# Kernel optimization log

Measured on AMD Instinct MI355X. Metric: run time of the kernel, lower is better.

Reference implementation:

```python
import jax, jax.numpy as jnp
import numpy as np

N, H, NH, E = 1024, 128, 8, 32768
DH = H // NH


def setup_inputs() -> dict:
    key = jax.random.key(0)
    ks = jax.random.split(key, 8)
    scale = 0.02
    return {
        "x": jax.random.normal(ks[0], (N, H), jnp.float32),
        "edge_index": jax.random.randint(ks[1], (2, E), 0, N, dtype=jnp.int32),
        "edge_attr": jax.random.normal(ks[2], (E, H), jnp.float32),
        "batch": jnp.zeros((N,), jnp.int32),
        "in_proj_w": jax.random.normal(ks[3], (3 * H, H), jnp.float32) * scale,
        "in_proj_b": jax.random.normal(ks[4], (3 * H,), jnp.float32) * scale,
        "out_w": jax.random.normal(ks[5], (H, H), jnp.float32) * scale,
        "out_b": jax.random.normal(ks[6], (H,), jnp.float32) * scale,
    }


def reference(x, edge_index, edge_attr, batch, in_proj_w, in_proj_b, out_w, out_b):
    # batch is all-zeros (single graph), matching the module's .squeeze(0) usage.
    n, h = x.shape
    src, dst = edge_index[0], edge_index[1]

    # to_dense_adj with edge_attr: dense key [S=N, B=N, H]; duplicates sum (scatter-add)
    key_dense = jnp.zeros((n, n, h), x.dtype).at[src, dst].add(edge_attr)
    # adjacency for the key_padding_mask; diagonal forced unmasked
    adjacency = jnp.zeros((n, n), x.dtype).at[src, dst].add(1.0)
    mask = (adjacency == 0) & (~jnp.eye(n, dtype=bool))  # [B=N, S=N], True = masked

    wq, wk, wv = in_proj_w[:h], in_proj_w[h:2 * h], in_proj_w[2 * h:]
    bq, bk, bv = in_proj_b[:h], in_proj_b[h:2 * h], in_proj_b[2 * h:]

    q = (x @ wq.T + bq).reshape(n, NH, DH)                 # [B, nh, dh]
    k = (key_dense @ wk.T + bk).reshape(n, n, NH, DH)      # [S, B, nh, dh]
    v = (key_dense @ wv.T + bv).reshape(n, n, NH, DH)      # [S, B, nh, dh]

    scores = jnp.einsum('bnd,sbnd->bns', q, k) * (1.0 / np.sqrt(DH))  # [B, nh, S]
    scores = jnp.where(mask[:, None, :], -jnp.inf, scores)
    attn = jax.nn.softmax(scores, axis=-1)

    out = jnp.einsum('bns,sbnd->bnd', attn, v).reshape(n, h)
    return out @ out_w.T + out_b
```

## Files before the change

### kernel.cpp

```cpp
#include <hip/hip_runtime.h>

#define NN 1024
#define HD 128
#define NHEAD 8
#define DHEAD 16
#define NE 32768
#define MAXDEG 128
#define PRE 16


__global__ __launch_bounds__(256) void bucket_kernel(
    const int* __restrict__ src, const int* __restrict__ dst,
    int* __restrict__ cntIn, unsigned int* __restrict__ adjBit,
    int* __restrict__ byDst) {
  int e = blockIdx.x * 256 + threadIdx.x;
  int s = src[e], d = dst[e];
  atomicOr(&adjBit[s * 32 + (d >> 5)], 1u << (d & 31));
  int si = atomicAdd(&cntIn[d << 4], 1);
  if (si < MAXDEG) byDst[d * MAXDEG + si] = (s << 16) | e;
}

__global__ __launch_bounds__(128) void node_kernel(
    const float* __restrict__ x, const float* __restrict__ ea,
    const float* __restrict__ W, const float* __restrict__ bias,
    const float* __restrict__ Wo, const float* __restrict__ ob,
    const int* __restrict__ cntIn, const unsigned int* __restrict__ adjBit,
    const int* __restrict__ byDst, float* __restrict__ out) {
  const int b = blockIdx.x, t = threadIdx.x;
  const int w = t >> 6, lane = t & 63;
  const int hn = lane >> 3, hc = lane & 7;

  __shared__ float xs[HD], qs[HD], aos[HD];
  __shared__ float qks[NHEAD * 136];
  __shared__ unsigned int aw[32];
  __shared__ int eList[MAXDEG];
  __shared__ unsigned short ePos[MAXDEG];
  __shared__ short fIdx[MAXDEG];
  __shared__ float eDot[MAXDEG * NHEAD];
  __shared__ float eAttn[MAXDEG * NHEAD];
  __shared__ float qbv[NHEAD];
  __shared__ int nSurv, allowedCnt, ndCnt;

  if (t < 32) aw[t] = adjBit[b * 32 + t];
  if (t == 0) { nSurv = 0; ndCnt = 0; }
  xs[t] = x[(size_t)b * HD + t];
  const int degI = min(cntIn[b << 4], MAXDEG);
  __syncthreads();
  if (t == 0) aw[b >> 5] |= 1u << (b & 31);
  __syncthreads();
  if (t < 32) {
    int pc = __popc(aw[t]);
    #pragma unroll
    for (int off = 16; off; off >>= 1) pc += __shfl_xor(pc, off, 32);
    if (t == 0) allowedCnt = pc;
  }

  if (t < degI) {
    int pk = byDst[b * MAXDEG + t];
    int e = pk & 0xFFFF, s = pk >> 16;
    if ((aw[s >> 5] >> (s & 31)) & 1) {
      int k = atomicAdd(&nSurv, 1);
      eList[k] = e; ePos[k] = (unsigned short)s;
    }
  }
  {
    const float4* wr = (const float4*)(W + (size_t)t * HD);
    const float4* xv4 = (const float4*)xs;
    float acc = bias[t];
    #pragma unroll
    for (int k = 0; k < HD / 4; k++) {
      float4 wv = wr[k]; float4 xv = xv4[k];
      acc += xv.x * wv.x + xv.y * wv.y + xv.z * wv.z + xv.w * wv.w;
    }
    qs[t] = acc;
    float p = acc * bias[HD + t];
    #pragma unroll
    for (int off = 8; off; off >>= 1) p += __shfl_xor(p, off, 16);
    if ((t & 15) == 0) qbv[t >> 4] = p;
  }
  __syncthreads();

  {
    const float4* wk4 = (const float4*)(W + HD * HD);
    const int c4 = t & 31, np = t >> 5;
    float4* qks4 = (float4*)qks;
    #pragma unroll
    for (int h = 0; h < 2; h++) {
      const int n = np + h * 4;
      float4 acc = make_float4(0.f, 0.f, 0.f, 0.f);
      #pragma unroll
      for (int d = 0; d < DHEAD; d++) {
        float qv = qs[n * DHEAD + d];
        float4 wv = wk4[(n * DHEAD + d) * 32 + c4];
        acc.x += qv * wv.x; acc.y += qv * wv.y;
        acc.z += qv * wv.z; acc.w += qv * wv.w;
      }
      qks4[n * 34 + c4] = acc;
    }
  }
  __syncthreads();
  const int ns = nSurv;

  float pre[PRE];
  #pragma unroll
  for (int k = 0; k < PRE; k++) {
    int e = (k < ns) ? eList[k] : 0;
    pre[k] = ea[(size_t)e * HD + t];
  }

  float frag[16];
  #pragma unroll
  for (int i = 0; i < 16; i++) frag[i] = qks[hn * 136 + hc * 16 + i];
  for (int k = w; k < ns; k += 2) {
    const float4* ap = (const float4*)(ea + (size_t)eList[k] * HD + hc * 16);
    float p = 0.f;
    #pragma unroll
    for (int i = 0; i < 4; i++) {
      float4 av = ap[i];
      p += av.x * frag[i * 4 + 0] + av.y * frag[i * 4 + 1] +
           av.z * frag[i * 4 + 2] + av.w * frag[i * 4 + 3];
    }
    p += __shfl_xor(p, 1);
    p += __shfl_xor(p, 2);
    p += __shfl_xor(p, 4);
    if (hc == 0) eDot[k * NHEAD + hn] = p;
  }
  __syncthreads();

  if (t < ns) {
    const int my = ePos[t];
    int f = t;
    for (int j = t - 1; j >= 0; j--)
      if (ePos[j] == my) f = j;
    fIdx[t] = (short)f;
    if (f == t) {
      atomicAdd(&ndCnt, 1);
    } else {
      #pragma unroll
      for (int n = 0; n < NHEAD; n++)
        atomicAdd(&eDot[f * NHEAD + n], eDot[t * NHEAD + n]);
    }
  }
  __syncthreads();

  {
    const int n = t >> 4, l16 = t & 15;
    const int nd = ndCnt;
    const float qb = qbv[n];
    const float sb = qb * 0.25f;
    float m = sb;
    for (int k = l16; k < ns; k += 16) {
      if (fIdx[k] == k) {
        float sc = (eDot[k * NHEAD + n] + qb) * 0.25f;
        eAttn[k * NHEAD + n] = sc;
        m = fmaxf(m, sc);
      }
    }
    #pragma unroll
    for (int off = 8; off; off >>= 1) m = fmaxf(m, __shfl_xor(m, off, 16));
    float l = 0.f;
    for (int k = l16; k < ns; k += 16)
      if (fIdx[k] == k) l += expf(eAttn[k * NHEAD + n] - m);
    #pragma unroll
    for (int off = 8; off; off >>= 1) l += __shfl_xor(l, off, 16);
    l += (float)(allowedCnt - nd) * expf(sb - m);
    const float inv = 1.0f / l;
    for (int k = l16; k < ns; k += 16)
      eDot[k * NHEAD + n] = expf(eAttn[fIdx[k] * NHEAD + n] - m) * inv;
  }
  __syncthreads();

  float aggr[NHEAD];
  #pragma unroll
  for (int n = 0; n < NHEAD; n++) aggr[n] = 0.f;
  #pragma unroll
  for (int k = 0; k < PRE; k++) {
    if (k < ns) {
      const float4* ed4 = (const float4*)&eDot[k * NHEAD];
      float4 a0 = ed4[0], a1 = ed4[1];
      float av = pre[k];
      aggr[0] += a0.x * av; aggr[1] += a0.y * av;
      aggr[2] += a0.z * av; aggr[3] += a0.w * av;
      aggr[4] += a1.x * av; aggr[5] += a1.y * av;
      aggr[6] += a1.z * av; aggr[7] += a1.w * av;
    }
  }
  for (int k = PRE; k < ns; k++) {
    float av = ea[(size_t)eList[k] * HD + t];
    #pragma unroll
    for (int n = 0; n < NHEAD; n++) aggr[n] += eDot[k * NHEAD + n] * av;
  }
  __syncthreads();
  #pragma unroll
  for (int n = 0; n < NHEAD; n++) qks[n * 136 + t] = aggr[n];
  __syncthreads();

  {
    int nj = t >> 4;
    const float4* wvr = (const float4*)(W + 2 * HD * HD + (size_t)t * HD);
    const float4* ar = (const float4*)&qks[nj * 136];
    float acc = bias[2 * HD + t];
    #pragma unroll
    for (int k = 0; k < HD / 4; k++) {
      float4 wv = wvr[k]; float4 av = ar[k];
      acc += av.x * wv.x + av.y * wv.y + av.z * wv.z + av.w * wv.w;
    }
    aos[t] = acc;
  }
  __syncthreads();
  {
    const float4* wor = (const float4*)(Wo + (size_t)t * HD);
    const float4* av4 = (const float4*)aos;
    float acc2 = ob[t];
    #pragma unroll
    for (int k = 0; k < HD / 4; k++) {
      float4 wv = wor[k]; float4 av = av4[k];
      acc2 += av.x * wv.x + av.y * wv.y + av.z * wv.z + av.w * wv.w;
    }
    out[(size_t)b * HD + t] = acc2;
  }
}

extern "C" void kernel_launch(void* const* d_in, const int* in_sizes, int n_in,
                              void* d_out, int out_size, void* d_ws, size_t ws_size,
                              hipStream_t stream) {
  const float* x     = (const float*)d_in[0];
  const int*   eidx  = (const int*)d_in[1];
  const float* eattr = (const float*)d_in[2];
  const float* in_w  = (const float*)d_in[4];
  const float* in_b  = (const float*)d_in[5];
  const float* out_w = (const float*)d_in[6];
  const float* out_b = (const float*)d_in[7];
  float* out = (float*)d_out;

  const int* src = eidx;
  const int* dst = eidx + NE;

  char* ws = (char*)d_ws;
  int* cntIn            = (int*)(ws + 0);
  unsigned int* adjBit  = (unsigned int*)(ws + 65536);
  int* byDst            = (int*)(ws + 196608);

  hipMemsetAsync(ws, 0, 196608, stream);
  bucket_kernel<<<NE / 256, 256, 0, stream>>>(src, dst, cntIn, adjBit, byDst);
  node_kernel<<<NN, 128, 0, stream>>>(x, eattr, in_w, in_b, out_w, out_b,
                                      cntIn, adjBit, byDst, out);
}
```

Before: 107.2 us.

## Precompute Q and Q·Wk per node tile in prep kernel alongside edge bucketing

The per-node Q projection, the q·bk bias term and the Q·Wk folded key vectors move out of node_kernel. They are now computed by extra blocks of the bucketing kernel, 16 nodes per block, so each weight row loaded is reused across the tile. node_kernel reads the precomputed qk fragments and qbv values from workspace, which removes two matvecs and two barriers from its critical path. The cost is extra global writes and reads of a 4 MB qk buffer and more register use in the prep blocks.

```diff
diff --git a/kernel.cpp b/kernel.cpp
--- a/kernel.cpp
+++ b/kernel.cpp
@@ -7,43 +7,122 @@
 #define NE 32768
 #define MAXDEG 128
 #define PRE 16
-
-
-__global__ __launch_bounds__(256) void bucket_kernel(
+#define PTILE 16
+
+
+__global__ __launch_bounds__(256) void prep_kernel(
     const int* __restrict__ src, const int* __restrict__ dst,
     int* __restrict__ cntIn, unsigned int* __restrict__ adjBit,
-    int* __restrict__ byDst) {
-  int e = blockIdx.x * 256 + threadIdx.x;
-  int s = src[e], d = dst[e];
-  atomicOr(&adjBit[s * 32 + (d >> 5)], 1u << (d & 31));
-  int si = atomicAdd(&cntIn[d << 4], 1);
-  if (si < MAXDEG) byDst[d * MAXDEG + si] = (s << 16) | e;
+    int* __restrict__ byDst, const float* __restrict__ x,
+    const float* __restrict__ W, const float* __restrict__ bias,
+    float* __restrict__ qkAll, float* __restrict__ qbvAll) {
+  const int t = threadIdx.x;
+  if (blockIdx.x < NE / 256) {
+    int e = blockIdx.x * 256 + t;
+    int s = src[e], d = dst[e];
+    atomicOr(&adjBit[s * 32 + (d >> 5)], 1u << (d & 31));
+    int si = atomicAdd(&cntIn[d << 4], 1);
+    if (si < MAXDEG) byDst[d * MAXDEG + si] = (s << 16) | e;
+    return;
+  }
+  const int node0 = (blockIdx.x - NE / 256) * PTILE;
+  __shared__ float xT[PTILE][HD];
+  __shared__ float qT[PTILE][HD + 1];
+
+  #pragma unroll
+  for (int i = 0; i < 8; i++) {
+    int idx = i * 256 + t;
+    xT[idx >> 7][idx & 127] = x[(size_t)(node0 + (idx >> 7)) * HD + (idx & 127)];
+  }
+  __syncthreads();
+
+  {
+    const int r = t & 127, jh = t >> 7;
+    const float4* wr = (const float4*)(W + (size_t)r * HD);
+    const float bq = bias[r];
+    float acc[8];
+    #pragma unroll
+    for (int j = 0; j < 8; j++) acc[j] = bq;
+    for (int k = 0; k < HD / 4; k++) {
+      float4 wv = wr[k];
+      #pragma unroll
+      for (int j = 0; j < 8; j++) {
+        const float4 xv = *(const float4*)&xT[jh * 8 + j][k * 4];
+        acc[j] += xv.x * wv.x + xv.y * wv.y + xv.z * wv.z + xv.w * wv.w;
+      }
+    }
+    #pragma unroll
+    for (int j = 0; j < 8; j++) qT[jh * 8 + j][r] = acc[j];
+  }
+  __syncthreads();
+
+  if (t < 128) {
+    const int j = t >> 3, n = t & 7;
+    float s = 0.f;
+    #pragma unroll
+    for (int d = 0; d < DHEAD; d++) s += qT[j][n * 16 + d] * bias[HD + n * 16 + d];
+    qbvAll[(node0 + j) * NHEAD + n] = s;
+  }
+
+  {
+    const int c4 = t & 31, n = t >> 5;
+    const float4* wk4 = (const float4*)(W + HD * HD);
+    float4 acc[PTILE];
+    #pragma unroll
+    for (int j = 0; j < PTILE; j++) acc[j] = make_float4(0.f, 0.f, 0.f, 0.f);
+    #pragma unroll
+    for (int d = 0; d < DHEAD; d++) {
+      float4 wv = wk4[(n * 16 + d) * 32 + c4];
+      #pragma unroll
+      for (int j = 0; j < PTILE; j++) {
+        float qv = qT[j][n * 16 + d];
+        acc[j].x += qv * wv.x; acc[j].y += qv * wv.y;
+        acc[j].z += qv * wv.z; acc[j].w += qv * wv.w;
+      }
+    }
+    #pragma unroll
+    for (int j = 0; j < PTILE; j++) {
+      float4* out4 = (float4*)(qkAll + (size_t)(node0 + j) * 1024 + n * 128);
+      out4[c4] = acc[j];
+    }
+  }
 }
 
 __global__ __launch_bounds__(128) void node_kernel(
-    const float* __restrict__ x, const float* __restrict__ ea,
+    const float* __restrict__ ea,
     const float* __restrict__ W, const float* __restrict__ bias,
     const float* __restrict__ Wo, const float* __restrict__ ob,
     const int* __restrict__ cntIn, const unsigned int* __restrict__ adjBit,
-    const int* __restrict__ byDst, float* __restrict__ out) {
+    const int* __restrict__ byDst, const float* __restrict__ qkAll,
+    const float* __restrict__ qbvAll, float* __restrict__ out) {
   const int b = blockIdx.x, t = threadIdx.x;
   const int w = t >> 6, lane = t & 63;
   const int hn = lane >> 3, hc = lane & 7;
 
-  __shared__ float xs[HD], qs[HD], aos[HD];
-  __shared__ float qks[NHEAD * 136];
+  __shared__ float aos[HD];
+  __shared__ float aggS[NHEAD][136];
   __shared__ unsigned int aw[32];
   __shared__ int eList[MAXDEG];
   __shared__ unsigned short ePos[MAXDEG];
   __shared__ short fIdx[MAXDEG];
   __shared__ float eDot[MAXDEG * NHEAD];
   __shared__ float eAttn[MAXDEG * NHEAD];
-  __shared__ float qbv[NHEAD];
+  __shared__ float qbvS[NHEAD];
   __shared__ int nSurv, allowedCnt, ndCnt;
 
+  float frag[16];
+  {
+    const float4* qp = (const float4*)(qkAll + (size_t)b * 1024 + hn * 128 + hc * 16);
+    #pragma unroll
+    for (int i = 0; i < 4; i++) {
+      float4 v = qp[i];
+      frag[i * 4 + 0] = v.x; frag[i * 4 + 1] = v.y;
+      frag[i * 4 + 2] = v.z; frag[i * 4 + 3] = v.w;
+    }
+  }
+  if (t < NHEAD) qbvS[t] = qbvAll[b * NHEAD + t];
   if (t < 32) aw[t] = adjBit[b * 32 + t];
   if (t == 0) { nSurv = 0; ndCnt = 0; }
-  xs[t] = x[(size_t)b * HD + t];
   const int degI = min(cntIn[b << 4], MAXDEG);
   __syncthreads();
   if (t == 0) aw[b >> 5] |= 1u << (b & 31);
@@ -54,7 +133,6 @@
     for (int off = 16; off; off >>= 1) pc += __shfl_xor(pc, off, 32);
     if (t == 0) allowedCnt = pc;
   }
-
   if (t < degI) {
     int pk = byDst[b * MAXDEG + t];
     int e = pk & 0xFFFF, s = pk >> 16;
@@ -63,41 +141,6 @@
       eList[k] = e; ePos[k] = (unsigned short)s;
     }
   }
-  {
-    const float4* wr = (const float4*)(W + (size_t)t * HD);
-    const float4* xv4 = (const float4*)xs;
-    float acc = bias[t];
-    #pragma unroll
-    for (int k = 0; k < HD / 4; k++) {
-      float4 wv = wr[k]; float4 xv = xv4[k];
-      acc += xv.x * wv.x + xv.y * wv.y + xv.z * wv.z + xv.w * wv.w;
-    }
-    qs[t] = acc;
-    float p = acc * bias[HD + t];
-    #pragma unroll
-    for (int off = 8; off; off >>= 1) p += __shfl_xor(p, off, 16);
-    if ((t & 15) == 0) qbv[t >> 4] = p;
-  }
-  __syncthreads();
-
-  {
-    const float4* wk4 = (const float4*)(W + HD * HD);
-    const int c4 = t & 31, np = t >> 5;
-    float4* qks4 = (float4*)qks;
-    #pragma unroll
-    for (int h = 0; h < 2; h++) {
-      const int n = np + h * 4;
-      float4 acc = make_float4(0.f, 0.f, 0.f, 0.f);
-      #pragma unroll
-      for (int d = 0; d < DHEAD; d++) {
-        float qv = qs[n * DHEAD + d];
-        float4 wv = wk4[(n * DHEAD + d) * 32 + c4];
-        acc.x += qv * wv.x; acc.y += qv * wv.y;
-        acc.z += qv * wv.z; acc.w += qv * wv.w;
-      }
-      qks4[n * 34 + c4] = acc;
-    }
-  }
   __syncthreads();
   const int ns = nSurv;
 
@@ -108,9 +151,6 @@
     pre[k] = ea[(size_t)e * HD + t];
   }
 
-  float frag[16];
-  #pragma unroll
-  for (int i = 0; i < 16; i++) frag[i] = qks[hn * 136 + hc * 16 + i];
   for (int k = w; k < ns; k += 2) {
     const float4* ap = (const float4*)(ea + (size_t)eList[k] * HD + hc * 16);
     float p = 0.f;
@@ -146,7 +186,7 @@
   {
     const int n = t >> 4, l16 = t & 15;
     const int nd = ndCnt;
-    const float qb = qbv[n];
+    const float qb = qbvS[n];
     const float sb = qb * 0.25f;
     float m = sb;
     for (int k = l16; k < ns; k += 16) {
@@ -190,15 +230,14 @@
     #pragma unroll
     for (int n = 0; n < NHEAD; n++) aggr[n] += eDot[k * NHEAD + n] * av;
   }
-  __syncthreads();
-  #pragma unroll
-  for (int n = 0; n < NHEAD; n++) qks[n * 136 + t] = aggr[n];
+  #pragma unroll
+  for (int n = 0; n < NHEAD; n++) aggS[n][t] = aggr[n];
   __syncthreads();
 
   {
     int nj = t >> 4;
     const float4* wvr = (const float4*)(W + 2 * HD * HD + (size_t)t * HD);
-    const float4* ar = (const float4*)&qks[nj * 136];
+    const float4* ar = (const float4*)&aggS[nj][0];
     float acc = bias[2 * HD + t];
     #pragma unroll
     for (int k = 0; k < HD / 4; k++) {
@@ -240,9 +279,12 @@
   int* cntIn            = (int*)(ws + 0);
   unsigned int* adjBit  = (unsigned int*)(ws + 65536);
   int* byDst            = (int*)(ws + 196608);
+  float* qkAll          = (float*)(ws + 720896);
+  float* qbvAll         = (float*)(ws + 4915200);
 
   hipMemsetAsync(ws, 0, 196608, stream);
-  bucket_kernel<<<NE / 256, 256, 0, stream>>>(src, dst, cntIn, adjBit, byDst);
-  node_kernel<<<NN, 128, 0, stream>>>(x, eattr, in_w, in_b, out_w, out_b,
-                                      cntIn, adjBit, byDst, out);
+  prep_kernel<<<NE / 256 + NN / PTILE, 256, 0, stream>>>(
+      src, dst, cntIn, adjBit, byDst, x, in_w, in_b, qkAll, qbvAll);
+  node_kernel<<<NN, 128, 0, stream>>>(eattr, in_w, in_b, out_w, out_b,
+                                      cntIn, adjBit, byDst, qkAll, qbvAll, out);
 }
```

After: 107.4 us. About the same (+0.2%).
